# Kernel tuning notes

Measured on AMD Instinct MI355X. Metric: run time of the kernel, lower is better.

Reference implementation:

```python
import jax, jax.numpy as jnp
import numpy as np

ALPHA = 0.2  # LeakyReLU negative slope
NEG = -9e15


def _gat_heads(x, adj_mask, W, a):
    # x: (B,N,F); W: (H,F,O); a: (H,2O); adj_mask: (B,N,N) bool
    O = W.shape[-1]
    Wh = jnp.einsum('bnf,hfo->bhno', x, W)            # (B,H,N,O)
    e1 = jnp.einsum('bhno,ho->bhn', Wh, a[:, :O])     # Wh @ a[:O]
    e2 = jnp.einsum('bhno,ho->bhn', Wh, a[:, O:])     # Wh @ a[O:]
    e = jax.nn.leaky_relu(e1[:, :, :, None] + e2[:, :, None, :], ALPHA)  # (B,H,N,N)
    e = jnp.where(adj_mask[:, None], e, NEG)
    attn = jax.nn.softmax(e, axis=-1)
    return jnp.einsum('bhnm,bhmo->bhno', attn, Wh)    # (B,H,N,O)


def _gat_block(x, adj_mask, non_pad_mask, W_heads, a_heads, W_out, a_out):
    # multi-head layer, concat=True -> elu per head, then concat on feature dim
    h = jax.nn.elu(_gat_heads(x, adj_mask, W_heads, a_heads))  # (B,H,N,O)
    B, H, N, O = h.shape
    h = jnp.transpose(h, (0, 2, 1, 3)).reshape(B, N, H * O)
    h = h * non_pad_mask
    # out layer: single head, concat=False (no inner elu)
    h = _gat_heads(h, adj_mask, W_out[None], a_out[None])[:, 0]  # (B,N,noutput)
    h = h * non_pad_mask
    return jax.nn.elu(h)


def setup_inputs() -> dict:
    key = jax.random.key(0)
    ks = jax.random.split(key, 8)
    B, N = 32, 256
    vocab, F, O, H, OUT = 200, 300, 256, 8, 512
    fea = jax.random.randint(ks[0], (B, N), 0, vocab, dtype=jnp.int32)
    adj = jax.random.randint(ks[1], (B, N, N), 0, 2, dtype=jnp.int32)
    non_pad_mask = jnp.ones((B, N, 1), dtype=jnp.float32)
    embed = jax.random.normal(ks[2], (vocab, F), dtype=jnp.float32)
    W_heads = jax.random.normal(ks[3], (H, F, O), dtype=jnp.float32) / np.sqrt(F)
    a_heads = jax.random.normal(ks[4], (H, 2 * O), dtype=jnp.float32) / np.sqrt(2 * O)
    W_out = jax.random.normal(ks[5], (H * O, OUT), dtype=jnp.float32) / np.sqrt(H * O)
    a_out = jax.random.normal(ks[6], (2 * OUT,), dtype=jnp.float32) / np.sqrt(2 * OUT)
    return {"fea": fea, "adj": adj, "non_pad_mask": non_pad_mask, "embed": embed,
            "W_heads": W_heads, "a_heads": a_heads, "W_out": W_out, "a_out": a_out}


def reference(fea, adj, non_pad_mask, embed, W_heads, a_heads, W_out, a_out):
    adj_mask = adj > 0
    x = embed[fea]  # (B,N,F)
    # GAT_num = 1; dropout is identity in eval mode
    x = _gat_block(x, adj_mask, non_pad_mask, W_heads, a_heads, W_out, a_out)
    return x  # (B, N, 512)
```

## Files before the change

kernel.cpp:

```cpp
#include <hip/hip_runtime.h>
#include <math.h>


typedef _Float16 f16;
typedef __attribute__((ext_vector_type(8))) _Float16 f16x8;
typedef __attribute__((ext_vector_type(4))) _Float16 f16x4;
typedef __attribute__((ext_vector_type(4))) float f32x4;

__device__ __forceinline__ void async16(const void* g, void* lds) {
  __builtin_amdgcn_global_load_lds(
      (const __attribute__((address_space(1))) void*)g,
      (__attribute__((address_space(3))) void*)lds, 16, 0, 0);
}

__global__ __launch_bounds__(256) void k_prep(const int* __restrict__ fea,
                                              const float* __restrict__ embed,
                                              const float* __restrict__ Whd,
                                              const float* __restrict__ Wo,
                                              f16* __restrict__ x16,
                                              f16* __restrict__ WcT,
                                              f16* __restrict__ WoT,
                                              float* __restrict__ e_all) {
  int bid = blockIdx.x, tid = threadIdx.x;
  if (bid < 1280) {
    int idx = bid * 256 + tid;
    int row = idx / 40, c = idx % 40;
    int tok = fea[row];
    const float* eb = embed + (size_t)tok * 300;
    f16x8 v;
#pragma unroll
    for (int j = 0; j < 8; ++j) {
      int t = c * 8 + j;
      v[j] = (f16)((t < 300) ? eb[t] : 0.f);
    }
    *(f16x8*)&x16[(size_t)row * 320 + c * 8] = v;
  } else if (bid < 1920) {
    int r = bid - 1280;
    int zi = r * 256 + tid;
    if (zi < 16384) e_all[zi] = 0.f;
    __shared__ float tile[32][33];
    int bx = r % 10, q0 = r / 10;
    int by = q0 % 8, h = q0 / 8;
    int c = tid & 31, q = tid >> 5;
#pragma unroll
    for (int i = 0; i < 4; ++i) {
      int tt = q + i * 8;
      int t = bx * 32 + tt;
      float v = (t < 300) ? Whd[((size_t)h * 300 + t) * 256 + by * 32 + c] : 0.f;
      tile[tt][c] = v;
    }
    __syncthreads();
#pragma unroll
    for (int i = 0; i < 4; ++i) {
      int oo = q + i * 8;
      int gc = h * 256 + by * 32 + oo;
      WcT[(size_t)gc * 320 + bx * 32 + c] = (f16)tile[c][oo];
    }
  } else {
    int r = bid - 1920;
    __shared__ float tile[32][33];
    int bx = r % 64, by = r / 64;
    int c = tid & 31, q = tid >> 5;
#pragma unroll
    for (int i = 0; i < 4; ++i) {
      int kk = q + i * 8;
      tile[kk][c] = Wo[((size_t)bx * 32 + kk) * 512 + by * 32 + c];
    }
    __syncthreads();
#pragma unroll
    for (int i = 0; i < 4; ++i) {
      int oo = q + i * 8;
      WoT[((size_t)by * 32 + oo) * 2048 + bx * 32 + c] = (f16)tile[c][oo];
    }
  }
}

__global__ __launch_bounds__(512, 1) void k_l1(
    const f16* __restrict__ x16, const f16* __restrict__ WcT,
    const float* __restrict__ ah, const int* __restrict__ adj,
    const float* __restrict__ npm, f16* __restrict__ h1) {
  extern __shared__ __align__(16) char smem[];
  f16* As = (f16*)smem;
  f16* Bs = (f16*)(smem + 32768);
  char* WhB = smem;
  char* PB  = smem + 131072;
  float* e1f = (float*)(smem + 147456);
  float* e2f = (float*)(smem + 148480);

  const int bid = blockIdx.x;
  const int h = (bid >> 3) & 7;
  const int b = (bid & 7) * 4 + (bid >> 6);
  const int tid = threadIdx.x;
  const int wave = tid >> 6, lane = tid & 63;
  const int wm = wave >> 2, wn = wave & 3;
  const int lrow = lane & 15, quad = lane >> 4;
  const int srow = lane >> 3;
  const int scol = ((lane & 7) ^ (lane >> 3)) * 8;
  const int l7 = lrow & 7;

  if (tid < 256) e1f[tid] = 0.f;
  else e2f[tid - 256] = 0.f;

  f32x4 acc[8][4] = {};
  const f16* Ag = x16 + (size_t)b * 256 * 320;
  const f16* Bg = WcT + (size_t)h * 256 * 320;

  for (int t = 0; t < 5; ++t) {
    const int k0 = t * 64;
    __syncthreads();
#pragma unroll
    for (int j = 0; j < 4; ++j) {
      const int r0 = wave * 32 + j * 8;
      async16(Ag + (size_t)(r0 + srow) * 320 + k0 + scol, &As[r0 * 64]);
      async16(Bg + (size_t)(r0 + srow) * 320 + k0 + scol, &Bs[r0 * 64]);
    }
    __syncthreads();
#pragma unroll
    for (int s = 0; s < 2; ++s) {
      const int sq = ((s * 4 + quad) ^ l7) * 8;
      f16x8 af[8], bf[4];
#pragma unroll
      for (int mt = 0; mt < 8; ++mt)
        af[mt] = *(const f16x8*)&As[(wm * 128 + mt * 16 + lrow) * 64 + sq];
#pragma unroll
      for (int nt = 0; nt < 4; ++nt)
        bf[nt] = *(const f16x8*)&Bs[(wn * 64 + nt * 16 + lrow) * 64 + sq];
#pragma unroll
      for (int mt = 0; mt < 8; ++mt)
#pragma unroll
        for (int nt = 0; nt < 4; ++nt)
          acc[mt][nt] = __builtin_amdgcn_mfma_f32_16x16x32_f16(af[mt], bf[nt], acc[mt][nt], 0, 0, 0);
    }
  }
  __syncthreads();

  float a1v[4], a2v[4];
#pragma unroll
  for (int nt = 0; nt < 4; ++nt) {
    const int o = wn * 64 + nt * 16 + lrow;
    a1v[nt] = ah[h * 512 + o];
    a2v[nt] = ah[h * 512 + 256 + o];
  }
#pragma unroll
  for (int mt = 0; mt < 8; ++mt) {
    const int n0 = wm * 128 + mt * 16 + quad * 4;
    const int q16 = n0 >> 3;
    const int hoff = (n0 & 4) ? 8 : 0;
    float s1[4] = {0.f, 0.f, 0.f, 0.f}, s2[4] = {0.f, 0.f, 0.f, 0.f};
#pragma unroll
    for (int nt = 0; nt < 4; ++nt) {
      const int o = wn * 64 + nt * 16 + lrow;
      f16x4 v;
#pragma unroll
      for (int r = 0; r < 4; ++r) {
        v[r] = (f16)acc[mt][nt][r];
        s1[r] += acc[mt][nt][r] * a1v[nt];
        s2[r] += acc[mt][nt][r] * a2v[nt];
      }
      *(f16x4*)(WhB + o * 512 + ((q16 ^ (o & 7)) * 16 + hoff)) = v;
    }
#pragma unroll
    for (int r = 0; r < 4; ++r)
#pragma unroll
      for (int m = 1; m < 16; m <<= 1) {
        s1[r] += __shfl_xor(s1[r], m);
        s2[r] += __shfl_xor(s2[r], m);
      }
    if (lrow == 0) {
#pragma unroll
      for (int r = 0; r < 4; ++r) {
        atomicAdd(&e1f[n0 + r], s1[r]);
        atomicAdd(&e2f[n0 + r], s2[r]);
      }
    }
  }
  __syncthreads();

  float4 e2v = *(const float4*)&e2f[lane * 4];
  float e2m = fmaxf(fmaxf(e2v.x, e2v.y), fmaxf(e2v.z, e2v.w));
#pragma unroll
  for (int m = 1; m < 64; m <<= 1) e2m = fmaxf(e2m, __shfl_xor(e2m, m));

  for (int c = 0; c < 8; ++c) {
#pragma unroll
    for (int i = 0; i < 4; ++i) {
      int rl = i * 8 + wave;
      int n = c * 32 + rl;
      int gn = b * 256 + n;
      float er = e1f[n];
      float sh = er + e2m;
      sh = sh > 0.f ? sh : 0.2f * sh;
      int4 aj = *(const int4*)&adj[(size_t)gn * 256 + lane * 4];
      float p0, p1, p2, p3;
      {
        float v = er + e2v.x; v = v > 0.f ? v : 0.2f * v;
        p0 = aj.x ? __expf(v - sh) : 0.f;
        v = er + e2v.y; v = v > 0.f ? v : 0.2f * v;
        p1 = aj.y ? __expf(v - sh) : 0.f;
        v = er + e2v.z; v = v > 0.f ? v : 0.2f * v;
        p2 = aj.z ? __expf(v - sh) : 0.f;
        v = er + e2v.w; v = v > 0.f ? v : 0.2f * v;
        p3 = aj.w ? __expf(v - sh) : 0.f;
      }
      float sm = p0 + p1 + p2 + p3;
#pragma unroll
      for (int m = 1; m < 64; m <<= 1) sm += __shfl_xor(sm, m);
      float rs = 1.f / sm;
      f16x4 pw;
      pw[0] = (f16)(p0 * rs); pw[1] = (f16)(p1 * rs);
      pw[2] = (f16)(p2 * rs); pw[3] = (f16)(p3 * rs);
      *(f16x4*)(PB + rl * 512 + (((lane >> 1) ^ (rl & 7)) * 16 + (lane & 1) * 8)) = pw;
    }
    __syncthreads();

    f32x4 acc2[2][2] = {};
#pragma unroll
    for (int kk = 0; kk < 8; ++kk) {
      f16x8 af2[2], bf2[2];
#pragma unroll
      for (int mtO = 0; mtO < 2; ++mtO) {
        int o = wave * 32 + mtO * 16 + lrow;
        af2[mtO] = *(const f16x8*)(WhB + o * 512 + (((kk * 4 + quad) ^ (o & 7)) * 16));
      }
#pragma unroll
      for (int ntN = 0; ntN < 2; ++ntN) {
        int rl = ntN * 16 + lrow;
        bf2[ntN] = *(const f16x8*)(PB + rl * 512 + (((kk * 4 + quad) ^ (rl & 7)) * 16));
      }
#pragma unroll
      for (int mtO = 0; mtO < 2; ++mtO)
#pragma unroll
        for (int ntN = 0; ntN < 2; ++ntN)
          acc2[mtO][ntN] = __builtin_amdgcn_mfma_f32_16x16x32_f16(af2[mtO], bf2[ntN], acc2[mtO][ntN], 0, 0, 0);
    }
    __syncthreads();

#pragma unroll
    for (int ntN = 0; ntN < 2; ++ntN) {
      int n = c * 32 + ntN * 16 + lrow;
      int gn = b * 256 + n;
      float pm = npm[gn];
#pragma unroll
      for (int mtO = 0; mtO < 2; ++mtO) {
        int o0 = wave * 32 + mtO * 16 + quad * 4;
        f16x4 st;
#pragma unroll
        for (int r = 0; r < 4; ++r) {
          float v = acc2[mtO][ntN][r];
          v = v > 0.f ? v : (__expf(v) - 1.f);
          st[r] = (f16)(v * pm);
        }
        *(f16x4*)&h1[(size_t)gn * 2048 + h * 256 + o0] = st;
      }
    }
  }
}

__global__ __launch_bounds__(256, 4) void k_gemm_sk(const f16* __restrict__ A,
                                                    const f16* __restrict__ BT,
                                                    f16* __restrict__ outSK,
                                                    const float* __restrict__ ao,
                                                    float* __restrict__ e12,
                                                    float* __restrict__ e22) {
  __shared__ f16 As[128 * 64];
  __shared__ f16 Bs[64 * 64];
  const int by = blockIdx.x, bx = blockIdx.y, kz = blockIdx.z;
  const int tid = threadIdx.x;
  const int wave = tid >> 6, lane = tid & 63;
  const int wm = wave >> 1, wn = wave & 1;
  const int lrow = lane & 15, quad = lane >> 4;
  const int srow = lane >> 3;
  const int scol = ((lane & 7) ^ (lane >> 3)) * 8;
  const int l7 = lrow & 7;

  f32x4 acc[4][2] = {};
  const f16* Ag = A + (size_t)by * 128 * 2048;
  const f16* Bg = BT + (size_t)bx * 64 * 2048;
  const int kbeg = kz * 1024;

  for (int k0 = kbeg; k0 < kbeg + 1024; k0 += 64) {
    __syncthreads();
#pragma unroll
    for (int j = 0; j < 4; ++j) {
      const int r0 = wave * 32 + j * 8;
      async16(Ag + (size_t)(r0 + srow) * 2048 + k0 + scol, &As[r0 * 64]);
    }
#pragma unroll
    for (int j = 0; j < 2; ++j) {
      const int r0 = wave * 16 + j * 8;
      async16(Bg + (size_t)(r0 + srow) * 2048 + k0 + scol, &Bs[r0 * 64]);
    }
    __syncthreads();
#pragma unroll
    for (int s = 0; s < 2; ++s) {
      const int sq = ((s * 4 + quad) ^ l7) * 8;
      f16x8 af[4], bf[2];
#pragma unroll
      for (int t = 0; t < 4; ++t)
        af[t] = *(const f16x8*)&As[(wm * 64 + t * 16 + lrow) * 64 + sq];
#pragma unroll
      for (int t = 0; t < 2; ++t)
        bf[t] = *(const f16x8*)&Bs[(wn * 32 + t * 16 + lrow) * 64 + sq];
#pragma unroll
      for (int mt = 0; mt < 4; ++mt)
#pragma unroll
        for (int nt = 0; nt < 2; ++nt)
          acc[mt][nt] = __builtin_amdgcn_mfma_f32_16x16x32_f16(af[mt], bf[nt], acc[mt][nt], 0, 0, 0);
    }
  }

  const int b = (by * 128) >> 8;
  const int nbase0 = (by * 128) & 255;
  f16* dst = outSK + (size_t)kz * 32 * 512 * 256;
#pragma unroll
  for (int mt = 0; mt < 4; ++mt) {
    const int nb = nbase0 + wm * 64 + mt * 16 + quad * 4;
#pragma unroll
    for (int nt = 0; nt < 2; ++nt) {
      const int gc = bx * 64 + wn * 32 + nt * 16 + lrow;
      f16x4 v;
#pragma unroll
      for (int r = 0; r < 4; ++r) v[r] = (f16)acc[mt][nt][r];
      *(f16x4*)&dst[((size_t)b * 512 + gc) * 256 + nb] = v;
    }
  }

  float a1v[2], a2v[2];
#pragma unroll
  for (int nt = 0; nt < 2; ++nt) {
    const int gc = bx * 64 + wn * 32 + nt * 16 + lrow;
    a1v[nt] = ao[gc];
    a2v[nt] = ao[512 + gc];
  }
#pragma unroll
  for (int mt = 0; mt < 4; ++mt) {
    float s1[4] = {0.f, 0.f, 0.f, 0.f}, s2[4] = {0.f, 0.f, 0.f, 0.f};
#pragma unroll
    for (int nt = 0; nt < 2; ++nt)
#pragma unroll
      for (int r = 0; r < 4; ++r) {
        s1[r] += acc[mt][nt][r] * a1v[nt];
        s2[r] += acc[mt][nt][r] * a2v[nt];
      }
#pragma unroll
    for (int r = 0; r < 4; ++r)
#pragma unroll
      for (int m = 1; m < 16; m <<= 1) {
        s1[r] += __shfl_xor(s1[r], m);
        s2[r] += __shfl_xor(s2[r], m);
      }
    if (lrow == 0) {
      const int nb = nbase0 + wm * 64 + mt * 16 + quad * 4;
#pragma unroll
      for (int r = 0; r < 4; ++r) {
        atomicAdd(&e12[b * 256 + nb + r], s1[r]);
        atomicAdd(&e22[b * 256 + nb + r], s2[r]);
      }
    }
  }
}

#define PSTRIDE 264

__global__ __launch_bounds__(256, 4) void k_attn2(
    const f16* __restrict__ sk, const float* __restrict__ e1g, const float* __restrict__ e2g,
    const int* __restrict__ adj, const float* __restrict__ npm, float* __restrict__ out) {
  int bid = blockIdx.x;
  int nt0 = (bid >> 3) & 3;
  int pair = (bid >> 5) * 8 + (bid & 7);
  int oh = pair >> 5, b = pair & 31;
  int n0 = nt0 * 64;
  __shared__ f16 P[64 * PSTRIDE];
  int tid = threadIdx.x;
  int wave = tid >> 6, lane = tid & 63;

  float4 e2v = *(const float4*)&e2g[b * 256 + lane * 4];
  float e2m = fmaxf(fmaxf(e2v.x, e2v.y), fmaxf(e2v.z, e2v.w));
#pragma unroll
  for (int m = 1; m < 64; m <<= 1) e2m = fmaxf(e2m, __shfl_xor(e2m, m));
#pragma unroll 4
  for (int i = 0; i < 16; ++i) {
    int row = i * 4 + wave;
    int gn = b * 256 + n0 + row;
    float er = e1g[b * 256 + n0 + row];
    float sh = er + e2m;
    sh = sh > 0.f ? sh : 0.2f * sh;
    int4 aj = *(const int4*)&adj[(size_t)gn * 256 + lane * 4];
    float p0, p1, p2, p3;
    {
      float v = er + e2v.x; v = v > 0.f ? v : 0.2f * v;
      p0 = aj.x ? __expf(v - sh) : 0.f;
      v = er + e2v.y; v = v > 0.f ? v : 0.2f * v;
      p1 = aj.y ? __expf(v - sh) : 0.f;
      v = er + e2v.z; v = v > 0.f ? v : 0.2f * v;
      p2 = aj.z ? __expf(v - sh) : 0.f;
      v = er + e2v.w; v = v > 0.f ? v : 0.2f * v;
      p3 = aj.w ? __expf(v - sh) : 0.f;
    }
    float sm = p0 + p1 + p2 + p3;
#pragma unroll
    for (int m = 1; m < 64; m <<= 1) sm += __shfl_xor(sm, m);
    float rs = 1.f / sm;
    f16x4 pw;
    pw[0] = (f16)(p0 * rs); pw[1] = (f16)(p1 * rs);
    pw[2] = (f16)(p2 * rs); pw[3] = (f16)(p3 * rs);
    *(f16x4*)&P[row * PSTRIDE + lane * 4] = pw;
  }
  __syncthreads();

  int lrow = lane & 15, quad = lane >> 4;
  f32x4 acc[2][4] = {};
  const f16* Ag0 = sk + ((size_t)b * 512 + oh * 128) * 256;
  const f16* Ag1 = Ag0 + (size_t)32 * 512 * 256;
#pragma unroll 2
  for (int k0 = 0; k0 < 256; k0 += 32) {
    f16x8 af[2], bf[4];
#pragma unroll
    for (int mt = 0; mt < 2; ++mt) {
      size_t off = (size_t)(wave * 32 + mt * 16 + lrow) * 256 + k0 + quad * 8;
      af[mt] = *(const f16x8*)&Ag0[off] + *(const f16x8*)&Ag1[off];
    }
#pragma unroll
    for (int nt = 0; nt < 4; ++nt)
      bf[nt] = *(const f16x8*)&P[(nt * 16 + lrow) * PSTRIDE + k0 + quad * 8];
#pragma unroll
    for (int mt = 0; mt < 2; ++mt)
#pragma unroll
      for (int nt = 0; nt < 4; ++nt)
        acc[mt][nt] = __builtin_amdgcn_mfma_f32_16x16x32_f16(af[mt], bf[nt], acc[mt][nt], 0, 0, 0);
  }
#pragma unroll
  for (int nt = 0; nt < 4; ++nt) {
    int nloc = nt * 16 + lrow;
    int gn = b * 256 + n0 + nloc;
    float pm = npm[gn];
#pragma unroll
    for (int mt = 0; mt < 2; ++mt) {
      int o0 = oh * 128 + wave * 32 + mt * 16 + quad * 4;
      float4 st;
      float v0 = acc[mt][nt][0] * pm;
      float v1 = acc[mt][nt][1] * pm;
      float v2 = acc[mt][nt][2] * pm;
      float v3 = acc[mt][nt][3] * pm;
      st.x = v0 > 0.f ? v0 : (__expf(v0) - 1.f);
      st.y = v1 > 0.f ? v1 : (__expf(v1) - 1.f);
      st.z = v2 > 0.f ? v2 : (__expf(v2) - 1.f);
      st.w = v3 > 0.f ? v3 : (__expf(v3) - 1.f);
      *(float4*)&out[(size_t)gn * 512 + o0] = st;
    }
  }
}

extern "C" void kernel_launch(void* const* d_in, const int* in_sizes, int n_in,
                              void* d_out, int out_size, void* d_ws, size_t ws_size,
                              hipStream_t stream) {
  (void)in_sizes; (void)n_in; (void)out_size; (void)ws_size;
  const int*   fea   = (const int*)d_in[0];
  const int*   adj   = (const int*)d_in[1];
  const float* npm   = (const float*)d_in[2];
  const float* embed = (const float*)d_in[3];
  const float* Whd   = (const float*)d_in[4];
  const float* ah    = (const float*)d_in[5];
  const float* Wo    = (const float*)d_in[6];
  const float* ao    = (const float*)d_in[7];
  float* out = (float*)d_out;

  char* ws = (char*)d_ws;
  f16* x16  = (f16*)ws;  ws += (size_t)8192 * 320 * 2;
  f16* WcT  = (f16*)ws;  ws += (size_t)2048 * 320 * 2;
  f16* WoT  = (f16*)ws;  ws += (size_t)512 * 2048 * 2;
  f16* h1   = (f16*)ws;  ws += (size_t)8192 * 2048 * 2;
  f16* Wh2sk = (f16*)ws; ws += (size_t)2 * 32 * 512 * 256 * 2;
  float* e12 = (float*)ws; ws += (size_t)8192 * 4;
  float* e22 = (float*)ws; ws += (size_t)8192 * 4;

  k_prep<<<2944, 256, 0, stream>>>(fea, embed, Whd, Wo, x16, WcT, WoT, e12);

  k_l1<<<256, 512, 149504, stream>>>(x16, WcT, ah, adj, npm, h1);

  k_gemm_sk<<<dim3(64, 8, 2), 256, 0, stream>>>(h1, WoT, Wh2sk, ao, e12, e22);
  k_attn2<<<512, 256, 0, stream>>>(Wh2sk, e12, e22, adj, npm, out);
}
```

Baseline: 191.6 us.

## Double k_l1 block to 1024 threads and pack adjacency rows into LDS bitmasks

The fused layer-1 kernel now runs 16 waves per block instead of 8, so each wave owns half as many MFMA tiles in both the projection GEMM and the attention-times-Wh GEMM. This cuts per-thread register pressure and adds latency hiding. During the K loop, the adjacency rows for the batch are read once, converted with ballot into 64-bit masks, and stored in LDS, so the softmax phase reads bits instead of reloading int4 adjacency from global memory. This costs extra LDS, more threads per barrier, and a 1024-thread block that may restrict register allocation.

```diff
diff --git a/kernel.cpp b/kernel.cpp
--- a/kernel.cpp
+++ b/kernel.cpp
@@ -6,6 +6,7 @@
 typedef __attribute__((ext_vector_type(8))) _Float16 f16x8;
 typedef __attribute__((ext_vector_type(4))) _Float16 f16x4;
 typedef __attribute__((ext_vector_type(4))) float f32x4;
+typedef unsigned long long u64;
 
 __device__ __forceinline__ void async16(const void* g, void* lds) {
   __builtin_amdgcn_global_load_lds(
@@ -75,7 +76,7 @@
   }
 }
 
-__global__ __launch_bounds__(512, 1) void k_l1(
+__global__ __launch_bounds__(1024, 1) void k_l1(
     const f16* __restrict__ x16, const f16* __restrict__ WcT,
     const float* __restrict__ ah, const int* __restrict__ adj,
     const float* __restrict__ npm, f16* __restrict__ h1) {
@@ -86,6 +87,7 @@
   char* PB  = smem + 131072;
   float* e1f = (float*)(smem + 147456);
   float* e2f = (float*)(smem + 148480);
+  u64* adjB = (u64*)(smem + 149504);
 
   const int bid = blockIdx.x;
   const int h = (bid >> 3) & 7;
@@ -99,34 +101,50 @@
   const int l7 = lrow & 7;
 
   if (tid < 256) e1f[tid] = 0.f;
-  else e2f[tid - 256] = 0.f;
-
-  f32x4 acc[8][4] = {};
+  else if (tid < 512) e2f[tid - 256] = 0.f;
+
+  f32x4 acc[4][4] = {};
   const f16* Ag = x16 + (size_t)b * 256 * 320;
   const f16* Bg = WcT + (size_t)h * 256 * 320;
+  const int* adjRow = adj + (size_t)b * 256 * 256;
 
   for (int t = 0; t < 5; ++t) {
     const int k0 = t * 64;
     __syncthreads();
 #pragma unroll
-    for (int j = 0; j < 4; ++j) {
-      const int r0 = wave * 32 + j * 8;
+    for (int j = 0; j < 2; ++j) {
+      const int r0 = wave * 16 + j * 8;
       async16(Ag + (size_t)(r0 + srow) * 320 + k0 + scol, &As[r0 * 64]);
       async16(Bg + (size_t)(r0 + srow) * 320 + k0 + scol, &Bs[r0 * 64]);
     }
+    if (t < 4) {
+#pragma unroll
+      for (int i = 0; i < 4; ++i) {
+        int row = wave * 16 + t * 4 + i;
+        const int* ar = adjRow + (size_t)row * 256;
+        u64 m0 = __ballot(ar[lane] != 0);
+        u64 m1 = __ballot(ar[64 + lane] != 0);
+        u64 m2 = __ballot(ar[128 + lane] != 0);
+        u64 m3 = __ballot(ar[192 + lane] != 0);
+        if (lane == 0) adjB[row * 4 + 0] = m0;
+        if (lane == 16) adjB[row * 4 + 1] = m1;
+        if (lane == 32) adjB[row * 4 + 2] = m2;
+        if (lane == 48) adjB[row * 4 + 3] = m3;
+      }
+    }
     __syncthreads();
 #pragma unroll
     for (int s = 0; s < 2; ++s) {
       const int sq = ((s * 4 + quad) ^ l7) * 8;
-      f16x8 af[8], bf[4];
-#pragma unroll
-      for (int mt = 0; mt < 8; ++mt)
-        af[mt] = *(const f16x8*)&As[(wm * 128 + mt * 16 + lrow) * 64 + sq];
+      f16x8 af[4], bf[4];
+#pragma unroll
+      for (int mt = 0; mt < 4; ++mt)
+        af[mt] = *(const f16x8*)&As[(wm * 64 + mt * 16 + lrow) * 64 + sq];
 #pragma unroll
       for (int nt = 0; nt < 4; ++nt)
         bf[nt] = *(const f16x8*)&Bs[(wn * 64 + nt * 16 + lrow) * 64 + sq];
 #pragma unroll
-      for (int mt = 0; mt < 8; ++mt)
+      for (int mt = 0; mt < 4; ++mt)
 #pragma unroll
         for (int nt = 0; nt < 4; ++nt)
           acc[mt][nt] = __builtin_amdgcn_mfma_f32_16x16x32_f16(af[mt], bf[nt], acc[mt][nt], 0, 0, 0);
@@ -142,8 +160,8 @@
     a2v[nt] = ah[h * 512 + 256 + o];
   }
 #pragma unroll
-  for (int mt = 0; mt < 8; ++mt) {
-    const int n0 = wm * 128 + mt * 16 + quad * 4;
+  for (int mt = 0; mt < 4; ++mt) {
+    const int n0 = wm * 64 + mt * 16 + quad * 4;
     const int q16 = n0 >> 3;
     const int hoff = (n0 & 4) ? 8 : 0;
     float s1[4] = {0.f, 0.f, 0.f, 0.f}, s2[4] = {0.f, 0.f, 0.f, 0.f};
@@ -183,24 +201,24 @@
 
   for (int c = 0; c < 8; ++c) {
 #pragma unroll
-    for (int i = 0; i < 4; ++i) {
-      int rl = i * 8 + wave;
+    for (int i = 0; i < 2; ++i) {
+      int rl = i * 16 + wave;
       int n = c * 32 + rl;
-      int gn = b * 256 + n;
       float er = e1f[n];
       float sh = er + e2m;
       sh = sh > 0.f ? sh : 0.2f * sh;
-      int4 aj = *(const int4*)&adj[(size_t)gn * 256 + lane * 4];
+      u64 mrow = adjB[n * 4 + (lane >> 4)];
+      int bits = (int)((mrow >> ((lane & 15) * 4)) & 0xFull);
       float p0, p1, p2, p3;
       {
         float v = er + e2v.x; v = v > 0.f ? v : 0.2f * v;
-        p0 = aj.x ? __expf(v - sh) : 0.f;
+        p0 = (bits & 1) ? __expf(v - sh) : 0.f;
         v = er + e2v.y; v = v > 0.f ? v : 0.2f * v;
-        p1 = aj.y ? __expf(v - sh) : 0.f;
+        p1 = (bits & 2) ? __expf(v - sh) : 0.f;
         v = er + e2v.z; v = v > 0.f ? v : 0.2f * v;
-        p2 = aj.z ? __expf(v - sh) : 0.f;
+        p2 = (bits & 4) ? __expf(v - sh) : 0.f;
         v = er + e2v.w; v = v > 0.f ? v : 0.2f * v;
-        p3 = aj.w ? __expf(v - sh) : 0.f;
+        p3 = (bits & 8) ? __expf(v - sh) : 0.f;
       }
       float sm = p0 + p1 + p2 + p3;
 #pragma unroll
@@ -213,25 +231,17 @@
     }
     __syncthreads();
 
-    f32x4 acc2[2][2] = {};
+    f32x4 acc2[2] = {};
 #pragma unroll
     for (int kk = 0; kk < 8; ++kk) {
-      f16x8 af2[2], bf2[2];
-#pragma unroll
-      for (int mtO = 0; mtO < 2; ++mtO) {
-        int o = wave * 32 + mtO * 16 + lrow;
-        af2[mtO] = *(const f16x8*)(WhB + o * 512 + (((kk * 4 + quad) ^ (o & 7)) * 16));
-      }
+      int o = wave * 16 + lrow;
+      f16x8 af2 = *(const f16x8*)(WhB + o * 512 + (((kk * 4 + quad) ^ (o & 7)) * 16));
 #pragma unroll
       for (int ntN = 0; ntN < 2; ++ntN) {
         int rl = ntN * 16 + lrow;
-        bf2[ntN] = *(const f16x8*)(PB + rl * 512 + (((kk * 4 + quad) ^ (rl & 7)) * 16));
-      }
-#pragma unroll
-      for (int mtO = 0; mtO < 2; ++mtO)
-#pragma unroll
-        for (int ntN = 0; ntN < 2; ++ntN)
-          acc2[mtO][ntN] = __builtin_amdgcn_mfma_f32_16x16x32_f16(af2[mtO], bf2[ntN], acc2[mtO][ntN], 0, 0, 0);
+        f16x8 bf2 = *(const f16x8*)(PB + rl * 512 + (((kk * 4 + quad) ^ (rl & 7)) * 16));
+        acc2[ntN] = __builtin_amdgcn_mfma_f32_16x16x32_f16(af2, bf2, acc2[ntN], 0, 0, 0);
+      }
     }
     __syncthreads();
 
@@ -240,18 +250,15 @@
       int n = c * 32 + ntN * 16 + lrow;
       int gn = b * 256 + n;
       float pm = npm[gn];
-#pragma unroll
-      for (int mtO = 0; mtO < 2; ++mtO) {
-        int o0 = wave * 32 + mtO * 16 + quad * 4;
-        f16x4 st;
-#pragma unroll
-        for (int r = 0; r < 4; ++r) {
-          float v = acc2[mtO][ntN][r];
-          v = v > 0.f ? v : (__expf(v) - 1.f);
-          st[r] = (f16)(v * pm);
-        }
-        *(f16x4*)&h1[(size_t)gn * 2048 + h * 256 + o0] = st;
-      }
+      int o0 = wave * 16 + quad * 4;
+      f16x4 st;
+#pragma unroll
+      for (int r = 0; r < 4; ++r) {
+        float v = acc2[ntN][r];
+        v = v > 0.f ? v : (__expf(v) - 1.f);
+        st[r] = (f16)(v * pm);
+      }
+      *(f16x4*)&h1[(size_t)gn * 2048 + h * 256 + o0] = st;
     }
   }
 }
@@ -476,7 +483,7 @@
 
   k_prep<<<2944, 256, 0, stream>>>(fea, embed, Whd, Wo, x16, WcT, WoT, e12);
 
-  k_l1<<<256, 512, 149504, stream>>>(x16, WcT, ah, adj, npm, h1);
+  k_l1<<<256, 1024, 157696, stream>>>(x16, WcT, ah, adj, npm, h1);
 
   k_gemm_sk<<<dim3(64, 8, 2), 256, 0, stream>>>(h1, WoT, Wh2sk, ao, e12, e22);
   k_attn2<<<512, 256, 0, stream>>>(Wh2sk, e12, e22, adj, npm, out);
```

After: 207.5 us. 8.3% more time.

## Double-buffer layer-1 GEMM tiles and prefetch adjacency rows ahead of softmax

Applied to the files above, without the earlier changes.

The first GEMM's K loop in k_l1 now uses two LDS buffers. The next K tile is issued asynchronously while MFMAs run on the current one, which removes one barrier per iteration and the exposed load latency. The adjacency rows for each 32-row chunk are also loaded into registers one chunk ahead, so the global load overlaps the previous chunk's softmax and aggregation. The cost is higher register pressure from the extra int4 arrays, and the second LDS buffer reuses space that later phases also use.

```diff
diff --git a/kernel.cpp b/kernel.cpp
--- a/kernel.cpp
+++ b/kernel.cpp
@@ -80,8 +80,8 @@
     const float* __restrict__ ah, const int* __restrict__ adj,
     const float* __restrict__ npm, f16* __restrict__ h1) {
   extern __shared__ __align__(16) char smem[];
-  f16* As = (f16*)smem;
-  f16* Bs = (f16*)(smem + 32768);
+  f16* AsB[2] = {(f16*)smem, (f16*)(smem + 65536)};
+  f16* BsB[2] = {(f16*)(smem + 32768), (f16*)(smem + 98304)};
   char* WhB = smem;
   char* PB  = smem + 131072;
   float* e1f = (float*)(smem + 147456);
@@ -105,16 +105,29 @@
   const f16* Ag = x16 + (size_t)b * 256 * 320;
   const f16* Bg = WcT + (size_t)h * 256 * 320;
 
+#pragma unroll
+  for (int j = 0; j < 4; ++j) {
+    const int r0 = wave * 32 + j * 8;
+    async16(Ag + (size_t)(r0 + srow) * 320 + scol, &AsB[0][r0 * 64]);
+    async16(Bg + (size_t)(r0 + srow) * 320 + scol, &BsB[0][r0 * 64]);
+  }
+  __syncthreads();
+
+#pragma unroll
   for (int t = 0; t < 5; ++t) {
-    const int k0 = t * 64;
-    __syncthreads();
-#pragma unroll
-    for (int j = 0; j < 4; ++j) {
-      const int r0 = wave * 32 + j * 8;
-      async16(Ag + (size_t)(r0 + srow) * 320 + k0 + scol, &As[r0 * 64]);
-      async16(Bg + (size_t)(r0 + srow) * 320 + k0 + scol, &Bs[r0 * 64]);
-    }
-    __syncthreads();
+    const f16* As = AsB[t & 1];
+    const f16* Bs = BsB[t & 1];
+    if (t < 4) {
+      const int kn = (t + 1) * 64;
+      f16* An = AsB[(t + 1) & 1];
+      f16* Bn = BsB[(t + 1) & 1];
+#pragma unroll
+      for (int j = 0; j < 4; ++j) {
+        const int r0 = wave * 32 + j * 8;
+        async16(Ag + (size_t)(r0 + srow) * 320 + kn + scol, &An[r0 * 64]);
+        async16(Bg + (size_t)(r0 + srow) * 320 + kn + scol, &Bn[r0 * 64]);
+      }
+    }
 #pragma unroll
     for (int s = 0; s < 2; ++s) {
       const int sq = ((s * 4 + quad) ^ l7) * 8;
@@ -131,8 +144,14 @@
         for (int nt = 0; nt < 4; ++nt)
           acc[mt][nt] = __builtin_amdgcn_mfma_f32_16x16x32_f16(af[mt], bf[nt], acc[mt][nt], 0, 0, 0);
     }
-  }
-  __syncthreads();
+    __syncthreads();
+  }
+
+  const int* adjRow = adj + (size_t)b * 256 * 256;
+  int4 ajR[4], ajN[4];
+#pragma unroll
+  for (int i = 0; i < 4; ++i)
+    ajR[i] = *(const int4*)&adjRow[(size_t)(i * 8 + wave) * 256 + lane * 4];
 
   float a1v[4], a2v[4];
 #pragma unroll
@@ -182,15 +201,19 @@
   for (int m = 1; m < 64; m <<= 1) e2m = fmaxf(e2m, __shfl_xor(e2m, m));
 
   for (int c = 0; c < 8; ++c) {
+    if (c < 7) {
+#pragma unroll
+      for (int i = 0; i < 4; ++i)
+        ajN[i] = *(const int4*)&adjRow[(size_t)((c + 1) * 32 + i * 8 + wave) * 256 + lane * 4];
+    }
 #pragma unroll
     for (int i = 0; i < 4; ++i) {
       int rl = i * 8 + wave;
       int n = c * 32 + rl;
-      int gn = b * 256 + n;
       float er = e1f[n];
       float sh = er + e2m;
       sh = sh > 0.f ? sh : 0.2f * sh;
-      int4 aj = *(const int4*)&adj[(size_t)gn * 256 + lane * 4];
+      int4 aj = ajR[i];
       float p0, p1, p2, p3;
       {
         float v = er + e2v.x; v = v > 0.f ? v : 0.2f * v;
@@ -253,6 +276,8 @@
         *(f16x4*)&h1[(size_t)gn * 2048 + h * 256 + o0] = st;
       }
     }
+#pragma unroll
+    for (int i = 0; i < 4; ++i) ajR[i] = ajN[i];
   }
 }
 
```

After: 184.5 us. -3.7%, faster.
